# Kernel tuning notes

Measured on AMD Instinct MI355X. Metric: run time of the kernel, lower is better.

Reference implementation:

```python
import jax, jax.numpy as jnp
import numpy as np

N = 20000
E = 320000
IN_DIM = 256
OUT_DIM = 64
HEADS = 4
EDGE_DIM = 32
NEG_SLOPE = 0.2


def setup_inputs() -> dict:
    key = jax.random.key(0)
    ks = jax.random.split(key, 10)
    HD = HEADS * OUT_DIM
    x = jax.random.normal(ks[0], (N, IN_DIM), dtype=jnp.float32)
    edge_index = jax.random.randint(ks[1], (2, E), 0, N, dtype=jnp.int64)
    edge_attr = jax.random.normal(ks[2], (E, EDGE_DIM), dtype=jnp.float32)
    # xavier_uniform with gain sqrt(2)
    def xavier(k, shape):
        fan_in, fan_out = shape[1], shape[0]
        a = np.sqrt(2.0) * np.sqrt(6.0 / (fan_in + fan_out))
        return jax.random.uniform(k, shape, jnp.float32, -a, a)
    lin_W = xavier(ks[3], (HD, IN_DIM))          # [H*D, in_dim]
    att_src = xavier(ks[4], (HEADS, OUT_DIM))    # [H, D]
    att_dst = xavier(ks[5], (HEADS, OUT_DIM))
    lin_edge_W = xavier(ks[6], (HD, EDGE_DIM))
    att_edge = xavier(ks[7], (HEADS, OUT_DIM))
    bias = jnp.zeros((HD,), dtype=jnp.float32)
    return {"x": x, "edge_index": edge_index, "edge_attr": edge_attr,
            "lin_W": lin_W, "att_src": att_src, "att_dst": att_dst,
            "lin_edge_W": lin_edge_W, "att_edge": att_edge, "bias": bias}


def _gat_forward(x, edge_attr, lin_W, att_src, att_dst, lin_edge_W, att_edge, bias, edge_index):
    n = x.shape[0]
    # add self loops (static shapes)
    loops = jnp.arange(n, dtype=edge_index.dtype)
    ei = jnp.concatenate([edge_index, jnp.stack([loops, loops])], axis=1)  # [2, E+N]
    ea = jnp.concatenate([edge_attr, jnp.zeros((n, edge_attr.shape[1]), edge_attr.dtype)], axis=0)
    src, dst = ei[0], ei[1]
    # node projection: [N, H, D]
    x_proj = (x @ lin_W.T).reshape(n, HEADS, OUT_DIM)
    # per-node attention scores, then gather scalars per edge (avoids gathering x_dst)
    s_src = jnp.einsum('nhd,hd->nh', x_proj, att_src)  # [N, H]
    s_dst = jnp.einsum('nhd,hd->nh', x_proj, att_dst)
    att = s_src[src] + s_dst[dst]                      # [E', H]
    # edge feature contribution
    e_proj = (ea @ lin_edge_W.T).reshape(-1, HEADS, OUT_DIM)
    att = att + jnp.einsum('ehd,hd->eh', e_proj, att_edge)
    att = jnp.where(att >= 0, att, NEG_SLOPE * att)    # leaky_relu
    # segment softmax over dst (self-loops guarantee every node has >=1 edge)
    seg_max = jax.ops.segment_max(att, dst, num_segments=n)
    exps = jnp.exp(att - seg_max[dst])
    denom = jax.ops.segment_sum(exps, dst, num_segments=n)
    alpha = exps / (denom[dst] + 1e-12)               # [E', H]
    # messages and scatter-sum
    m = x_proj[src] * alpha[:, :, None]               # [E', H, D]
    out = jax.ops.segment_sum(m, dst, num_segments=n) # [N, H, D]
    out = out.reshape(n, HEADS * OUT_DIM) + bias
    return out


def reference(x, edge_index, edge_attr, lin_W, att_src, att_dst, lin_edge_W, att_edge, bias):
    return _gat_forward(x, edge_attr, lin_W, att_src, att_dst, lin_edge_W, att_edge, bias, edge_index)
```

## Files before the change

kernel.cpp:

```cpp
#include <hip/hip_runtime.h>
#include <math.h>

#define IN_DIM 256
#define HD 256
#define EDGE_DIM 32
#define NEG_SLOPE 0.2f
#define NTHR 256
#define WCVT_VBS 32

typedef _Float16 f16x8 __attribute__((ext_vector_type(8)));
typedef _Float16 f16x4 __attribute__((ext_vector_type(4)));
typedef float f32x4 __attribute__((ext_vector_type(4)));

__device__ __forceinline__ f16x8 cvt8(const float* p) {
    float4 lo = *(const float4*)p;
    float4 hi = *(const float4*)(p + 4);
    auto a = __builtin_amdgcn_cvt_pkrtz(lo.x, lo.y);
    auto b = __builtin_amdgcn_cvt_pkrtz(lo.z, lo.w);
    auto c = __builtin_amdgcn_cvt_pkrtz(hi.x, hi.y);
    auto d = __builtin_amdgcn_cvt_pkrtz(hi.z, hi.w);
    f16x8 r;
    r[0] = (_Float16)a[0]; r[1] = (_Float16)a[1];
    r[2] = (_Float16)b[0]; r[3] = (_Float16)b[1];
    r[4] = (_Float16)c[0]; r[5] = (_Float16)c[1];
    r[6] = (_Float16)d[0]; r[7] = (_Float16)d[1];
    return r;
}

__device__ __forceinline__ int detect64(const int* __restrict__ ei) {
    __shared__ int anynz;
    if (threadIdx.x == 0) anynz = 0;
    __syncthreads();
    if (ei[2 * threadIdx.x + 1] != 0) atomicOr(&anynz, 1);
    __syncthreads();
    return anynz == 0;
}

__device__ __forceinline__ void load_edge(const int* ei, int e, int E, int n, int is64,
                                          int& s, int& d) {
    if (e < E) {
        if (is64) { s = ei[2 * e]; d = ei[2 * E + 2 * e]; }
        else      { s = ei[e];     d = ei[E + e]; }
    } else {
        s = d = e - E;
    }
}

__global__ __launch_bounds__(NTHR) void k_pre(const float* __restrict__ lew,
                                              const float* __restrict__ ae,
                                              const float* __restrict__ W,
                                              float* __restrict__ weff,
                                              _Float16* __restrict__ Whr,
                                              int* __restrict__ deg, int n4) {
    int b = blockIdx.x;
    int t = threadIdx.x;
    if (b == 0) {
        if (t < 128) {
            int h = t >> 5, k = t & 31;
            float s = 0.f;
#pragma unroll 8
            for (int d = 0; d < 64; ++d) s += lew[(h * 64 + d) * 32 + k] * ae[h * 64 + d];
            weff[t] = s;
        }
    } else if (b <= WCVT_VBS) {
        int idx = (b - 1) * 2048 + t * 8;
        int col = idx >> 8;
        int k = idx & 255;
        f16x8 v = cvt8(&W[idx]);
        *(f16x8*)&Whr[(size_t)(k >> 3) * 2048 + col * 8] = v;
    } else {
        int i = (b - 1 - WCVT_VBS) * 1024 + t * 4;
        if (i < n4) *(int4*)&deg[i] = make_int4(0, 0, 0, 0);
    }
}

__global__ __launch_bounds__(NTHR) void k_hist(const int* __restrict__ ei,
                                               int* __restrict__ deg,
                                               int* __restrict__ perm, int E) {
    int is64 = detect64(ei);
    int e0 = (blockIdx.x * NTHR + threadIdx.x) * 4;
    if (e0 >= E) return;
    if (e0 + 4 <= E) {
        int4 pm;
        if (!is64) {
            int4 d4 = *(const int4*)&ei[E + e0];
            pm.x = atomicAdd(&deg[d4.x], 1);
            pm.y = atomicAdd(&deg[d4.y], 1);
            pm.z = atomicAdd(&deg[d4.z], 1);
            pm.w = atomicAdd(&deg[d4.w], 1);
        } else {
            int4 a = *(const int4*)&ei[2 * E + 2 * e0];
            int4 b4 = *(const int4*)&ei[2 * E + 2 * e0 + 4];
            pm.x = atomicAdd(&deg[a.x], 1);
            pm.y = atomicAdd(&deg[a.z], 1);
            pm.z = atomicAdd(&deg[b4.x], 1);
            pm.w = atomicAdd(&deg[b4.z], 1);
        }
        *(int4*)&perm[e0] = pm;
    } else {
        for (int e = e0; e < E && e < e0 + 4; ++e) {
            int d = is64 ? ei[2 * E + 2 * e] : ei[E + e];
            perm[e] = atomicAdd(&deg[d], 1);
        }
    }
}

#define XPLN 33
__global__ __launch_bounds__(NTHR) void k_proj(const float* __restrict__ x,
                                               const _Float16* __restrict__ Whr,
                                               const float* __restrict__ asrc_g,
                                               const float* __restrict__ adst_g,
                                               _Float16* __restrict__ xph,
                                               float* __restrict__ s_src,
                                               float* __restrict__ s_dst, int n) {
    __shared__ _Float16 xs[32 * XPLN * 8];
    int t = threadIdx.x;
    int lane = t & 63;
    int w = t >> 6;
    int m0 = blockIdx.x * 32;
    int c0 = w * 64;
    int r = lane & 15;
    int kq = lane >> 4;

    {
        int rr = t >> 3;
        int kc = (t & 7) * 32;
        int grow = m0 + rr;
        if (grow < n) {
            const float* xp = &x[(size_t)grow * IN_DIM + kc];
#pragma unroll
            for (int c4 = 0; c4 < 4; ++c4) {
                f16x8 v = cvt8(xp + c4 * 8);
                *(f16x8*)&xs[(size_t)((kc >> 3) + c4) * (XPLN * 8) + rr * 8] = v;
            }
        } else {
            f16x8 z = {0, 0, 0, 0, 0, 0, 0, 0};
#pragma unroll
            for (int c4 = 0; c4 < 4; ++c4)
                *(f16x8*)&xs[(size_t)((kc >> 3) + c4) * (XPLN * 8) + rr * 8] = z;
        }
    }

    float asr[4], ads[4];
#pragma unroll
    for (int ci = 0; ci < 4; ++ci) {
        asr[ci] = asrc_g[c0 + ci * 16 + r];
        ads[ci] = adst_g[c0 + ci * 16 + r];
    }

    f32x4 acc[2][4];
#pragma unroll
    for (int mi = 0; mi < 2; ++mi)
#pragma unroll
        for (int j = 0; j < 4; ++j) acc[mi][j] = (f32x4){0.f, 0.f, 0.f, 0.f};

    __syncthreads();

#pragma unroll
    for (int k0 = 0; k0 < IN_DIM; k0 += 32) {
        int p = (k0 >> 3) + kq;
        f16x8 a0 = *(const f16x8*)&xs[(size_t)p * (XPLN * 8) + (0 * 16 + r) * 8];
        f16x8 a1 = *(const f16x8*)&xs[(size_t)p * (XPLN * 8) + (1 * 16 + r) * 8];
        f16x8 bfr[4];
#pragma unroll
        for (int ci = 0; ci < 4; ++ci)
            bfr[ci] = *(const f16x8*)&Whr[(size_t)p * 2048 + (c0 + ci * 16 + r) * 8];
#pragma unroll
        for (int ci = 0; ci < 4; ++ci) {
            acc[0][ci] = __builtin_amdgcn_mfma_f32_16x16x32_f16(a0, bfr[ci], acc[0][ci],
                                                                0, 0, 0);
            acc[1][ci] = __builtin_amdgcn_mfma_f32_16x16x32_f16(a1, bfr[ci], acc[1][ci],
                                                                0, 0, 0);
        }
    }
#pragma unroll
    for (int mi = 0; mi < 2; ++mi) {
#pragma unroll
        for (int j = 0; j < 4; ++j) {
            int orow = m0 + mi * 16 + kq * 4 + j;
            if (orow < n) {
#pragma unroll
                for (int ci = 0; ci < 4; ++ci)
                    xph[(size_t)orow * HD + c0 + ci * 16 + r] = (_Float16)acc[mi][ci][j];
            }
        }
    }
#pragma unroll
    for (int mi = 0; mi < 2; ++mi) {
#pragma unroll
        for (int j = 0; j < 4; ++j) {
            float vs = 0.f, vd = 0.f;
#pragma unroll
            for (int ci = 0; ci < 4; ++ci) {
                vs += acc[mi][ci][j] * asr[ci];
                vd += acc[mi][ci][j] * ads[ci];
            }
#pragma unroll
            for (int msk = 1; msk < 16; msk <<= 1) {
                vs += __shfl_xor(vs, msk);
                vd += __shfl_xor(vd, msk);
            }
            int orow = m0 + mi * 16 + kq * 4 + j;
            if (r == 0 && orow < n) {
                s_src[orow * 4 + w] = vs;
                s_dst[orow * 4 + w] = vd;
            }
        }
    }
}

#define SCAN_T 1024
__global__ __launch_bounds__(SCAN_T) void scan_kernel(const int* __restrict__ deg,
                                                      int* __restrict__ rowptr, int n) {
    __shared__ int sdata[SCAN_T];
    int t = threadIdx.x;
    int per = (n + SCAN_T - 1) / SCAN_T;
    int begin = t * per;
    int endi = begin + per;
    if (endi > n) endi = n;
    if (begin > n) begin = n;
    bool vec = ((begin & 3) == 0) && (((endi - begin) & 3) == 0);
    int s = 0;
    if (vec) {
        for (int i = begin; i < endi; i += 4) {
            int4 v = *(const int4*)&deg[i];
            s += v.x + v.y + v.z + v.w + 4;
        }
    } else {
        for (int i = begin; i < endi; ++i) s += deg[i] + 1;
    }
    sdata[t] = s;
    __syncthreads();
    for (int off = 1; off < SCAN_T; off <<= 1) {
        int v = 0;
        if (t >= off) v = sdata[t - off];
        __syncthreads();
        sdata[t] += v;
        __syncthreads();
    }
    int run = (t == 0) ? 0 : sdata[t - 1];
    if (vec) {
        for (int i = begin; i < endi; i += 4) {
            int4 v = *(const int4*)&deg[i];
            int4 o;
            o.x = run; run += v.x + 1;
            o.y = run; run += v.y + 1;
            o.z = run; run += v.z + 1;
            o.w = run; run += v.w + 1;
            *(int4*)&rowptr[i] = o;
        }
    } else {
        for (int i = begin; i < endi; ++i) {
            rowptr[i] = run;
            run += deg[i] + 1;
        }
    }
    if (t == SCAN_T - 1) rowptr[n] = run;
}

__global__ __launch_bounds__(NTHR) void edge_kernel(const int* __restrict__ ei,
                                                    const float* __restrict__ ea,
                                                    const float* __restrict__ s_src,
                                                    const float* __restrict__ s_dst,
                                                    const float* __restrict__ weff,
                                                    const int* __restrict__ rowptr,
                                                    const int* __restrict__ perm,
                                                    int* __restrict__ src_csr,
                                                    float* __restrict__ p_csr,
                                                    int E, int n) {
    int is64 = detect64(ei);
    __shared__ float we[128];
    if (threadIdx.x < 128) we[threadIdx.x] = weff[threadIdx.x];
    __syncthreads();
    int e = blockIdx.x * blockDim.x + threadIdx.x;
    int EP = E + n;
    if (e >= EP) return;
    int s, d;
    load_edge(ei, e, E, n, is64, s, d);
    int pos;
    if (e < E) pos = rowptr[d] + perm[e];
    else       pos = rowptr[d + 1] - 1;
    float4 vs = *(const float4*)&s_src[(size_t)s * 4];
    float4 vd = *(const float4*)&s_dst[(size_t)d * 4];
    float ed[4] = {0.f, 0.f, 0.f, 0.f};
    if (e < E) {
#pragma unroll
        for (int k = 0; k < EDGE_DIM; k += 4) {
            float4 v = *(const float4*)&ea[(size_t)e * EDGE_DIM + k];
#pragma unroll
            for (int h = 0; h < 4; ++h) {
                ed[h] += v.x * we[h * 32 + k + 0] + v.y * we[h * 32 + k + 1] +
                         v.z * we[h * 32 + k + 2] + v.w * we[h * 32 + k + 3];
            }
        }
    }
    float t0 = vs.x + vd.x + ed[0];
    float t1 = vs.y + vd.y + ed[1];
    float t2 = vs.z + vd.z + ed[2];
    float t3 = vs.w + vd.w + ed[3];
    t0 = t0 >= 0.f ? t0 : NEG_SLOPE * t0;
    t1 = t1 >= 0.f ? t1 : NEG_SLOPE * t1;
    t2 = t2 >= 0.f ? t2 : NEG_SLOPE * t2;
    t3 = t3 >= 0.f ? t3 : NEG_SLOPE * t3;
    float4 o;
    o.x = __expf(t0);
    o.y = __expf(t1);
    o.z = __expf(t2);
    o.w = __expf(t3);
    src_csr[pos] = s;
    *(float4*)&p_csr[(size_t)pos * 4] = o;
}

__global__ __launch_bounds__(NTHR) void agg_kernel(const int* __restrict__ rowptr,
                                                   const int* __restrict__ src_csr,
                                                   const float* __restrict__ p_csr,
                                                   const _Float16* __restrict__ xph,
                                                   const float* __restrict__ bias,
                                                   float* __restrict__ out, int n) {
    int wid = (blockIdx.x * blockDim.x + threadIdx.x) >> 6;
    int lane = threadIdx.x & 63;
    if (wid >= n) return;
    int start = rowptr[wid];
    int end = rowptr[wid + 1];
    int h = lane >> 4;

    float dh = 0.f, ax = 0.f, ay = 0.f, az = 0.f, aw = 0.f;
    int i = start;
    for (; i + 8 <= end; i += 8) {
        int s_[8];
        float p_[8];
        f16x4 xv[8];
#pragma unroll
        for (int j = 0; j < 8; ++j) s_[j] = src_csr[i + j];
#pragma unroll
        for (int j = 0; j < 8; ++j) p_[j] = p_csr[(size_t)(i + j) * 4 + h];
#pragma unroll
        for (int j = 0; j < 8; ++j)
            xv[j] = *(const f16x4*)&xph[(size_t)s_[j] * HD + lane * 4];
#pragma unroll
        for (int j = 0; j < 8; ++j) {
            dh += p_[j];
            ax += p_[j] * (float)xv[j][0];
            ay += p_[j] * (float)xv[j][1];
            az += p_[j] * (float)xv[j][2];
            aw += p_[j] * (float)xv[j][3];
        }
    }
    for (; i < end; ++i) {
        int s0 = src_csr[i];
        float p0 = p_csr[(size_t)i * 4 + h];
        f16x4 x0 = *(const f16x4*)&xph[(size_t)s0 * HD + lane * 4];
        dh += p0;
        ax += p0 * (float)x0[0];
        ay += p0 * (float)x0[1];
        az += p0 * (float)x0[2];
        aw += p0 * (float)x0[3];
    }
    float invh = 1.f / (dh + 1e-12f);
    float4 b = *(const float4*)&bias[lane * 4];
    float4 o4;
    o4.x = ax * invh + b.x;
    o4.y = ay * invh + b.y;
    o4.z = az * invh + b.z;
    o4.w = aw * invh + b.w;
    *(float4*)&out[(size_t)wid * HD + lane * 4] = o4;
}

extern "C" void kernel_launch(void* const* d_in, const int* in_sizes, int n_in,
                              void* d_out, int out_size, void* d_ws, size_t ws_size,
                              hipStream_t stream) {
    const float* x        = (const float*)d_in[0];
    const int*   ei       = (const int*)d_in[1];
    const float* ea       = (const float*)d_in[2];
    const float* lin_W    = (const float*)d_in[3];
    const float* att_src  = (const float*)d_in[4];
    const float* att_dst  = (const float*)d_in[5];
    const float* lin_eW   = (const float*)d_in[6];
    const float* att_edge = (const float*)d_in[7];
    const float* bias     = (const float*)d_in[8];
    float* out = (float*)d_out;

    int n  = in_sizes[0] / IN_DIM;
    int E  = in_sizes[2] / EDGE_DIM;
    int EP = E + n;

    char* p = (char*)d_ws;
    auto alloc = [&](size_t bytes) {
        char* r = p;
        p += (bytes + 255) & ~(size_t)255;
        return r;
    };
    _Float16* xph   = (_Float16*)alloc((size_t)n * HD * 2);
    _Float16* Whr   = (_Float16*)alloc((size_t)HD * IN_DIM * 2);
    float* s_src    = (float*)alloc((size_t)n * 4 * 4);
    float* s_dst    = (float*)alloc((size_t)n * 4 * 4);
    float* p_csr    = (float*)alloc((size_t)EP * 4 * 4);
    float* weff     = (float*)alloc(128 * 4);
    int*   deg      = (int*)alloc((size_t)(n + 4) * 4);
    int*   rowptr   = (int*)alloc((size_t)(n + 1) * 4);
    int*   perm     = (int*)alloc((size_t)E * 4);
    int*   src_csr  = (int*)alloc((size_t)EP * 4);

    int n4 = (n + 3) & ~3;
    int ZV = (n4 + 1023) / 1024;

    k_pre<<<1 + WCVT_VBS + ZV, NTHR, 0, stream>>>(lin_eW, att_edge, lin_W, weff, Whr,
                                                  deg, n4);
    k_hist<<<(E + 1023) / 1024, NTHR, 0, stream>>>(ei, deg, perm, E);
    k_proj<<<(n + 31) / 32, NTHR, 0, stream>>>(x, Whr, att_src, att_dst, xph,
                                               s_src, s_dst, n);
    scan_kernel<<<1, SCAN_T, 0, stream>>>(deg, rowptr, n);
    edge_kernel<<<(EP + NTHR - 1) / NTHR, NTHR, 0, stream>>>(ei, ea, s_src, s_dst, weff,
                                                             rowptr, perm, src_csr, p_csr,
                                                             E, n);
    agg_kernel<<<(n + 3) / 4, NTHR, 0, stream>>>(rowptr, src_csr, p_csr, xph, bias, out, n);
}
```

Baseline: 98.37 us.

## Replace global-atomic degree histogram with per-block LDS histograms plus offset pass

```diff
diff --git a/kernel.cpp b/kernel.cpp
--- a/kernel.cpp
+++ b/kernel.cpp
@@ -7,6 +7,8 @@
 #define NEG_SLOPE 0.2f
 #define NTHR 256
 #define WCVT_VBS 32
+#define NB 128
+#define LDSW 10016
 
 typedef _Float16 f16x8 __attribute__((ext_vector_type(8)));
 typedef _Float16 f16x4 __attribute__((ext_vector_type(4)));
@@ -74,34 +76,57 @@
     }
 }
 
-__global__ __launch_bounds__(NTHR) void k_hist(const int* __restrict__ ei,
-                                               int* __restrict__ deg,
-                                               int* __restrict__ perm, int E) {
+__global__ __launch_bounds__(NTHR) void k_hist_lds(const int* __restrict__ ei,
+                                                   int* __restrict__ cnt_g,
+                                                   int* __restrict__ perm,
+                                                   int chunk, int E, int n) {
+    __shared__ int cnt_l[LDSW];
+    int b = blockIdx.x;
+    int t = threadIdx.x;
+    int is64 = detect64(ei);
+    int nw = (n + 1) >> 1;
+    for (int i = t; i < nw; i += NTHR) cnt_l[i] = 0;
+    __syncthreads();
+    int e0 = b * chunk;
+    int e1 = e0 + chunk;
+    if (e1 > E) e1 = E;
+    for (int e = e0 + t; e < e1; e += NTHR) {
+        int d = is64 ? ei[2 * E + 2 * e] : ei[E + e];
+        int sh = (d & 1) * 16;
+        int old = atomicAdd(&cnt_l[d >> 1], 1 << sh);
+        perm[e] = (old >> sh) & 0xffff;
+    }
+    __syncthreads();
+    for (int i = t; i < nw; i += NTHR) cnt_g[(size_t)b * nw + i] = cnt_l[i];
+}
+
+__global__ __launch_bounds__(NTHR) void k_h2(const int* __restrict__ cnt_g,
+                                             int* __restrict__ off_g,
+                                             int* __restrict__ deg, int n) {
+    int nw = (n + 1) >> 1;
+    int w = blockIdx.x * NTHR + threadIdx.x;
+    if (w >= nw) return;
+    int r0 = 0, r1 = 0;
+    for (int b = 0; b < NB; ++b) {
+        int v = cnt_g[(size_t)b * nw + w];
+        off_g[(size_t)b * n + 2 * w] = r0;
+        if (2 * w + 1 < n) off_g[(size_t)b * n + 2 * w + 1] = r1;
+        r0 += v & 0xffff;
+        r1 += (v >> 16) & 0xffff;
+    }
+    deg[2 * w] = r0;
+    if (2 * w + 1 < n) deg[2 * w + 1] = r1;
+}
+
+__global__ __launch_bounds__(NTHR) void k_hist_glb(const int* __restrict__ ei,
+                                                   int* __restrict__ deg,
+                                                   int* __restrict__ perm, int E) {
     int is64 = detect64(ei);
     int e0 = (blockIdx.x * NTHR + threadIdx.x) * 4;
     if (e0 >= E) return;
-    if (e0 + 4 <= E) {
-        int4 pm;
-        if (!is64) {
-            int4 d4 = *(const int4*)&ei[E + e0];
-            pm.x = atomicAdd(&deg[d4.x], 1);
-            pm.y = atomicAdd(&deg[d4.y], 1);
-            pm.z = atomicAdd(&deg[d4.z], 1);
-            pm.w = atomicAdd(&deg[d4.w], 1);
-        } else {
-            int4 a = *(const int4*)&ei[2 * E + 2 * e0];
-            int4 b4 = *(const int4*)&ei[2 * E + 2 * e0 + 4];
-            pm.x = atomicAdd(&deg[a.x], 1);
-            pm.y = atomicAdd(&deg[a.z], 1);
-            pm.z = atomicAdd(&deg[b4.x], 1);
-            pm.w = atomicAdd(&deg[b4.z], 1);
-        }
-        *(int4*)&perm[e0] = pm;
-    } else {
-        for (int e = e0; e < E && e < e0 + 4; ++e) {
-            int d = is64 ? ei[2 * E + 2 * e] : ei[E + e];
-            perm[e] = atomicAdd(&deg[d], 1);
-        }
+    for (int e = e0; e < E && e < e0 + 4; ++e) {
+        int d = is64 ? ei[2 * E + 2 * e] : ei[E + e];
+        perm[e] = atomicAdd(&deg[d], 1);
     }
 }
 
@@ -265,9 +290,10 @@
                                                     const float* __restrict__ weff,
                                                     const int* __restrict__ rowptr,
                                                     const int* __restrict__ perm,
+                                                    const int* __restrict__ off_g,
                                                     int* __restrict__ src_csr,
                                                     float* __restrict__ p_csr,
-                                                    int E, int n) {
+                                                    int chunk, int use_off, int E, int n) {
     int is64 = detect64(ei);
     __shared__ float we[128];
     if (threadIdx.x < 128) we[threadIdx.x] = weff[threadIdx.x];
@@ -278,8 +304,12 @@
     int s, d;
     load_edge(ei, e, E, n, is64, s, d);
     int pos;
-    if (e < E) pos = rowptr[d] + perm[e];
-    else       pos = rowptr[d + 1] - 1;
+    if (e < E) {
+        int extra = use_off ? off_g[(size_t)(e / chunk) * n + d] : 0;
+        pos = rowptr[d] + extra + perm[e];
+    } else {
+        pos = rowptr[d + 1] - 1;
+    }
     float4 vs = *(const float4*)&s_src[(size_t)s * 4];
     float4 vd = *(const float4*)&s_dst[(size_t)d * 4];
     float ed[4] = {0.f, 0.f, 0.f, 0.f};
@@ -383,6 +413,7 @@
     int n  = in_sizes[0] / IN_DIM;
     int E  = in_sizes[2] / EDGE_DIM;
     int EP = E + n;
+    int nw = (n + 1) >> 1;
 
     char* p = (char*)d_ws;
     auto alloc = [&](size_t bytes) {
@@ -400,18 +431,29 @@
     int*   rowptr   = (int*)alloc((size_t)(n + 1) * 4);
     int*   perm     = (int*)alloc((size_t)E * 4);
     int*   src_csr  = (int*)alloc((size_t)EP * 4);
+    int*   cnt_g    = (int*)alloc((size_t)NB * nw * 4);
+    int*   off_g    = (int*)alloc((size_t)NB * n * 4);
 
     int n4 = (n + 3) & ~3;
     int ZV = (n4 + 1023) / 1024;
+    int chunk = (E + NB - 1) / NB;
+    bool lds_ok = (n <= 2 * LDSW);
 
     k_pre<<<1 + WCVT_VBS + ZV, NTHR, 0, stream>>>(lin_eW, att_edge, lin_W, weff, Whr,
                                                   deg, n4);
-    k_hist<<<(E + 1023) / 1024, NTHR, 0, stream>>>(ei, deg, perm, E);
+    if (lds_ok) {
+        k_hist_lds<<<NB, NTHR, 0, stream>>>(ei, cnt_g, perm, chunk, E, n);
+    } else {
+        k_hist_glb<<<(E + 1023) / 1024, NTHR, 0, stream>>>(ei, deg, perm, E);
+    }
     k_proj<<<(n + 31) / 32, NTHR, 0, stream>>>(x, Whr, att_src, att_dst, xph,
                                                s_src, s_dst, n);
+    if (lds_ok) {
+        k_h2<<<(nw + NTHR - 1) / NTHR, NTHR, 0, stream>>>(cnt_g, off_g, deg, n);
+    }
     scan_kernel<<<1, SCAN_T, 0, stream>>>(deg, rowptr, n);
-    edge_kernel<<<(EP + NTHR - 1) / NTHR, NTHR, 0, stream>>>(ei, ea, s_src, s_dst, weff,
-                                                             rowptr, perm, src_csr, p_csr,
-                                                             E, n);
+    edge_kernel<<<(EP + NTHR - 1) / NTHR, NTHR, 0, stream>>>(
+        ei, ea, s_src, s_dst, weff, rowptr, perm, off_g, src_csr, p_csr,
+        chunk, lds_ok ? 1 : 0, E, n);
     agg_kernel<<<(n + 3) / 4, NTHR, 0, stream>>>(rowptr, src_csr, p_csr, xph, bias, out, n);
 }
```

After: 120.6 us. +22.6%, slower.
